# Performance work log

Measured on AMD Instinct MI355X. Metric: run time of the kernel, lower is better.

The kernel has to match this reference:

```python
import jax, jax.numpy as jnp
import numpy as np

N, F_NODE, F_FLOW, H, E, B, L = 131072, 64, 16, 128, 2097152, 256, 32


def setup_inputs() -> dict:
    key = jax.random.key(0)
    ks = jax.random.split(key, 24)
    gn = lambda k, s, sc: jax.random.normal(k, s, jnp.float32) * sc
    s_in = 1.0 / np.sqrt(F_NODE)
    s_h = 1.0 / np.sqrt(H)
    s_f = 1.0 / np.sqrt(F_FLOW)
    s_c = 1.0 / np.sqrt(2 * H + H // 2)
    inp = {
        "x": gn(ks[0], (N, F_NODE), 1.0),
        "edge_index": jax.random.randint(ks[1], (2, E), 0, N),
        "batch": jnp.sort(jax.random.randint(ks[2], (N,), 0, B)),
        "path_idx": jax.random.randint(ks[3], (B, L), 0, N),
        "path_len": jax.random.randint(ks[4], (B,), 1, L + 1),
        "flow": gn(ks[5], (B, F_FLOW), 1.0),
        # SAGEConv1: out = mean_agg(x_j) @ Wl.T + b + x_i @ Wr.T
        "Wl1": gn(ks[6], (H, F_NODE), s_in), "Wr1": gn(ks[7], (H, F_NODE), s_in), "b1": gn(ks[8], (H,), s_in),
        "Wl2": gn(ks[9], (H, H), s_h), "Wr2": gn(ks[10], (H, H), s_h), "b2": gn(ks[11], (H,), s_h),
        # LSTM (torch gate order i,f,g,o)
        "Wih": gn(ks[12], (4 * H, H), s_h), "Whh": gn(ks[13], (4 * H, H), s_h),
        "bih": gn(ks[14], (4 * H,), s_h), "bhh": gn(ks[15], (4 * H,), s_h),
        # flow encoder Linear(F_FLOW, H//2)
        "Wf": gn(ks[16], (H // 2, F_FLOW), s_f), "bf": gn(ks[17], (H // 2,), s_f),
        # scorer MLP: Linear(2H+H//2, H) -> ReLU -> Linear(H, 1)
        "Ws1": gn(ks[18], (H, 2 * H + H // 2), s_c), "bs1": gn(ks[19], (H,), s_c),
        "Ws2": gn(ks[20], (1, H), s_h), "bs2": gn(ks[21], (1,), s_h),
    }
    return inp


def _sage(x, src, dst, Wl, Wr, b, n):
    agg = jax.ops.segment_sum(x[src], dst, num_segments=n)  # [n, d]
    cnt = jax.ops.segment_sum(jnp.ones((src.shape[0],), x.dtype), dst, num_segments=n)
    mean = agg / jnp.maximum(cnt, 1.0)[:, None]
    return mean @ Wl.T + b + x @ Wr.T


def _lstm_final_h(seq, valid, Wih, Whh, bih, bhh):
    # seq: [B, L, H], valid: [B, L] bool; returns h at each path's last valid step
    b, l, h = seq.shape
    h0 = jnp.zeros((b, h), seq.dtype)

    def step(carry, inp):
        hp, cp = carry
        x_t, v = inp  # [B,H], [B]
        gates = x_t @ Wih.T + hp @ Whh.T + bih + bhh
        i, f, g, o = jnp.split(gates, 4, axis=-1)
        c_new = jax.nn.sigmoid(f) * cp + jax.nn.sigmoid(i) * jnp.tanh(g)
        h_new = jax.nn.sigmoid(o) * jnp.tanh(c_new)
        m = v[:, None]
        return (jnp.where(m, h_new, hp), jnp.where(m, c_new, cp)), None

    (hf, _), _ = jax.lax.scan(step, (h0, h0),
                              (jnp.swapaxes(seq, 0, 1), jnp.swapaxes(valid, 0, 1)))
    return hf


def reference(x, edge_index, batch, path_idx, path_len, flow,
              Wl1, Wr1, b1, Wl2, Wr2, b2,
              Wih, Whh, bih, bhh, Wf, bf, Ws1, bs1, Ws2, bs2):
    n = x.shape[0]
    src, dst = edge_index[0], edge_index[1]
    h1 = jax.nn.relu(_sage(x, src, dst, Wl1, Wr1, b1, n))
    node_emb = jax.nn.relu(_sage(h1, src, dst, Wl2, Wr2, b2, n))

    # global mean pool per graph
    gsum = jax.ops.segment_sum(node_emb, batch, num_segments=B)
    gcnt = jax.ops.segment_sum(jnp.ones((n,), node_emb.dtype), batch, num_segments=B)
    graph_emb = gsum / jnp.maximum(gcnt, 1.0)[:, None]  # [B, H]

    flow_emb = jax.nn.relu(flow @ Wf.T + bf)  # [B, H//2]

    path_seq = node_emb[path_idx]  # [B, L, H]
    valid = jnp.arange(L)[None, :] < path_len[:, None]  # [B, L]
    path_emb = _lstm_final_h(path_seq, valid, Wih, Whh, bih, bhh)  # [B, H]

    combined = jnp.concatenate([graph_emb, path_emb, flow_emb], axis=-1)
    hidden = jax.nn.relu(combined @ Ws1.T + bs1)
    scores = hidden @ Ws2.T + bs2  # [B, 1]
    return scores[:, 0]  # matches torch.cat of per-path [1] outputs -> [B]
```

## Files before the change

### kernel.cpp

```cpp
#include <hip/hip_runtime.h>
#include <hip/hip_bf16.h>

#define N_NODES 131072
#define N_EDGES 2097152
#define BATCHES 256
#define LPATH   32
#define NB   256
#define NPB  512
#define GB   256
#define EPB  8192

typedef __hip_bfloat16 bf16;
using short8  = __attribute__((ext_vector_type(8))) short;
using floatx4 = __attribute__((ext_vector_type(4))) float;

__device__ __forceinline__ float bl(unsigned u){ union {unsigned x; float f;} c; c.x = u << 16; return c.f; }
__device__ __forceinline__ float bh(unsigned u){ union {unsigned x; float f;} c; c.x = u & 0xffff0000u; return c.f; }
__device__ __forceinline__ unsigned packbf(float lo, float hi){
  bf16 l = __float2bfloat16(lo), h = __float2bfloat16(hi);
  unsigned short lu, hu;
  __builtin_memcpy(&lu, &l, 2); __builtin_memcpy(&hu, &h, 2);
  return (unsigned)lu | ((unsigned)hu << 16);
}
__device__ __forceinline__ float frcp(float x){ return __builtin_amdgcn_rcpf(x); }
__device__ __forceinline__ float sigf(float x){ return frcp(1.f + __expf(-x)); }
__device__ __forceinline__ float tanh_fast(float x){ return fmaf(2.f, frcp(1.f + __expf(-2.f * x)), -1.f); }

__global__ void prep_k(const float* __restrict__ Wl1, const float* __restrict__ Wr1,
                       const float* __restrict__ Wl2, const float* __restrict__ Wr2,
                       const float* __restrict__ Wih, const float* __restrict__ Whh,
                       const float* __restrict__ bih, const float* __restrict__ bhh,
                       bf16* __restrict__ Wcat1, bf16* __restrict__ Wcat2,
                       bf16* __restrict__ WihB, bf16* __restrict__ WhhB, float* __restrict__ bsumF){
  int g = blockIdx.x * 256 + threadIdx.x;
  if (g < 16384) {
    int h = g >> 7, k = g & 127;
    float v = (k < 64) ? Wl1[h * 64 + k] : Wr1[h * 64 + (k - 64)];
    Wcat1[g] = __float2bfloat16(v);
  } else if (g < 49152) {
    int q = g - 16384;
    int h = q >> 8, k = q & 255;
    float v = (k < 128) ? Wl2[h * 128 + k] : Wr2[h * 128 + (k - 128)];
    Wcat2[q] = __float2bfloat16(v);
  } else if (g < 114688) {
    int q = g - 49152;
    WihB[q] = __float2bfloat16(Wih[q]);
  } else if (g < 180224) {
    int q = g - 114688;
    WhhB[q] = __float2bfloat16(Whh[q]);
  } else if (g < 180736) {
    int k = g - 180224;
    bsumF[k] = bih[k] + bhh[k];
  }
}

__global__ void xb16_k(const float* __restrict__ x, bf16* __restrict__ xb, bf16* __restrict__ Acat1){
  int g = blockIdx.x * 256 + threadIdx.x;
  int n = g >> 5, p = g & 31;
  float2 v = *(const float2*)(x + (size_t)n * 64 + p * 2);
  unsigned u = packbf(v.x, v.y);
  *(unsigned*)(xb + (size_t)n * 64 + p * 2) = u;
  *(unsigned*)(Acat1 + (size_t)n * 128 + 64 + p * 2) = u;
}

__global__ void bounds_k(const int* __restrict__ batch, int* __restrict__ starts){
  int b = threadIdx.x;
  int lo = 0, hi = N_NODES;
  while (lo < hi){ int mid = (lo + hi) >> 1; if (batch[mid] < b) lo = mid + 1; else hi = mid; }
  starts[b] = lo;
  if (b == 0) starts[BATCHES] = N_NODES;
}

__global__ void cntA_k(const int* __restrict__ dst, int* __restrict__ cntA){
  __shared__ int h[NB];
  int tid = threadIdx.x;
  h[tid] = 0;
  __syncthreads();
  int base = blockIdx.x * EPB;
  #pragma unroll
  for (int i = 0; i < EPB / 256; ++i){
    int d = dst[base + i * 256 + tid];
    atomicAdd(&h[d >> 9], 1);
  }
  __syncthreads();
  cntA[tid * GB + blockIdx.x] = h[tid];
}

__global__ void scan1_k(const int* __restrict__ cnt, int* __restrict__ ofsA, int* __restrict__ bsum){
  __shared__ int sh[256];
  int t = threadIdx.x, i = blockIdx.x * 256 + t;
  int v = cnt[i];
  sh[t] = v; __syncthreads();
  int inc = v;
  for (int d = 1; d < 256; d <<= 1){
    int add = (t >= d) ? sh[t - d] : 0;
    __syncthreads();
    inc += add; sh[t] = inc;
    __syncthreads();
  }
  ofsA[i] = inc - v;
  if (t == 255) bsum[blockIdx.x] = inc;
}

__global__ void scan2_k(const int* __restrict__ bsum, int* __restrict__ bsumEx){
  __shared__ int sh[NB];
  int t = threadIdx.x;
  int v = bsum[t];
  sh[t] = v; __syncthreads();
  int inc = v;
  for (int d = 1; d < NB; d <<= 1){
    int add = (t >= d) ? sh[t - d] : 0;
    __syncthreads();
    inc += add; sh[t] = inc;
    __syncthreads();
  }
  bsumEx[t] = inc - v;
}

__global__ void passA2_k(const int* __restrict__ src, const int* __restrict__ dst,
                         const int* __restrict__ ofsA, const int* __restrict__ bsumEx,
                         unsigned* __restrict__ ebuf){
  __shared__ int cur[NB];
  int tid = threadIdx.x;
  cur[tid] = ofsA[tid * GB + blockIdx.x] + bsumEx[tid];
  __syncthreads();
  int base = blockIdx.x * EPB;
  #pragma unroll
  for (int i = 0; i < EPB / 256; ++i){
    int e = base + i * 256 + tid;
    int s = src[e], d = dst[e];
    int p = atomicAdd(&cur[d >> 9], 1);
    ebuf[p] = (unsigned)s | ((unsigned)(d & (NPB - 1)) << 17);
  }
}

__global__ void passB_k(const unsigned* __restrict__ ebuf, const int* __restrict__ bsumEx,
                        int* __restrict__ offs, int* __restrict__ srcS){
  __shared__ int ncnt[NPB];
  __shared__ int pairs[256];
  __shared__ int nofs[NPB];
  int k = blockIdx.x, tid = threadIdx.x;
  int bs = bsumEx[k];
  int be = (k < NB - 1) ? bsumEx[k + 1] : N_EDGES;
  ncnt[tid] = 0; ncnt[tid + 256] = 0;
  __syncthreads();
  for (int i = bs + tid; i < be; i += 256)
    atomicAdd(&ncnt[ebuf[i] >> 17], 1);
  __syncthreads();
  int p = ncnt[2 * tid] + ncnt[2 * tid + 1];
  pairs[tid] = p;
  __syncthreads();
  int inc = p;
  for (int d = 1; d < 256; d <<= 1){
    int add = (tid >= d) ? pairs[tid - d] : 0;
    __syncthreads();
    inc += add; pairs[tid] = inc;
    __syncthreads();
  }
  int ex = inc - p;
  nofs[2 * tid]     = ex;
  nofs[2 * tid + 1] = ex + ncnt[2 * tid];
  __syncthreads();
  offs[k * NPB + tid]       = bs + nofs[tid];
  offs[k * NPB + tid + 256] = bs + nofs[tid + 256];
  if (k == NB - 1 && tid == 0) offs[N_NODES] = N_EDGES;
  ncnt[tid] = nofs[tid]; ncnt[tid + 256] = nofs[tid + 256];
  __syncthreads();
  for (int i = bs + tid; i < be; i += 256){
    unsigned w = ebuf[i];
    int loc = w >> 17, sv = w & 0x1FFFF;
    int pp = atomicAdd(&ncnt[loc], 1);
    srcS[bs + pp] = sv;
  }
}

__global__ void agg1_k(const bf16* __restrict__ xb, const int* __restrict__ offs,
                       const int* __restrict__ srcS, bf16* __restrict__ Acat1){
  int wid = threadIdx.x >> 6, lane = threadIdx.x & 63;
  int n = blockIdx.x * 4 + wid;
  int s = offs[n], e = offs[n + 1];
  int slot = lane >> 3, fl = lane & 7;
  float a0=0,a1=0,a2=0,a3=0,a4=0,a5=0,a6=0,a7=0;
  float c0=0,c1=0,c2=0,c3=0,c4=0,c5=0,c6=0,c7=0;
  int i = s + slot;
  for (; i + 8 < e; i += 16){
    int sv0 = srcS[i], sv1 = srcS[i + 8];
    uint4 u = *(const uint4*)(xb + (size_t)sv0 * 64 + fl * 8);
    uint4 v = *(const uint4*)(xb + (size_t)sv1 * 64 + fl * 8);
    a0 += bl(u.x); a1 += bh(u.x); a2 += bl(u.y); a3 += bh(u.y);
    a4 += bl(u.z); a5 += bh(u.z); a6 += bl(u.w); a7 += bh(u.w);
    c0 += bl(v.x); c1 += bh(v.x); c2 += bl(v.y); c3 += bh(v.y);
    c4 += bl(v.z); c5 += bh(v.z); c6 += bl(v.w); c7 += bh(v.w);
  }
  if (i < e){
    int sv0 = srcS[i];
    uint4 u = *(const uint4*)(xb + (size_t)sv0 * 64 + fl * 8);
    a0 += bl(u.x); a1 += bh(u.x); a2 += bl(u.y); a3 += bh(u.y);
    a4 += bl(u.z); a5 += bh(u.z); a6 += bl(u.w); a7 += bh(u.w);
  }
  a0 += c0; a1 += c1; a2 += c2; a3 += c3;
  a4 += c4; a5 += c5; a6 += c6; a7 += c7;
  a0 += __shfl_xor(a0, 8); a0 += __shfl_xor(a0, 16); a0 += __shfl_xor(a0, 32);
  a1 += __shfl_xor(a1, 8); a1 += __shfl_xor(a1, 16); a1 += __shfl_xor(a1, 32);
  a2 += __shfl_xor(a2, 8); a2 += __shfl_xor(a2, 16); a2 += __shfl_xor(a2, 32);
  a3 += __shfl_xor(a3, 8); a3 += __shfl_xor(a3, 16); a3 += __shfl_xor(a3, 32);
  a4 += __shfl_xor(a4, 8); a4 += __shfl_xor(a4, 16); a4 += __shfl_xor(a4, 32);
  a5 += __shfl_xor(a5, 8); a5 += __shfl_xor(a5, 16); a5 += __shfl_xor(a5, 32);
  a6 += __shfl_xor(a6, 8); a6 += __shfl_xor(a6, 16); a6 += __shfl_xor(a6, 32);
  a7 += __shfl_xor(a7, 8); a7 += __shfl_xor(a7, 16); a7 += __shfl_xor(a7, 32);
  if (slot == 0){
    int d = e - s; if (d < 1) d = 1;
    float inv = 1.f / (float)d;
    uint4 w;
    w.x = packbf(a0 * inv, a1 * inv); w.y = packbf(a2 * inv, a3 * inv);
    w.z = packbf(a4 * inv, a5 * inv); w.w = packbf(a6 * inv, a7 * inv);
    *(uint4*)(Acat1 + (size_t)n * 128 + fl * 8) = w;
  }
}

__global__ void agg2_k(const int* __restrict__ offs, const int* __restrict__ srcS, bf16* __restrict__ Acat2){
  int wid = threadIdx.x >> 6, lane = threadIdx.x & 63;
  int n = blockIdx.x * 4 + wid;
  int s = offs[n], e = offs[n + 1];
  int slot = lane >> 4, fl = lane & 15;
  float a0=0,a1=0,a2=0,a3=0,a4=0,a5=0,a6=0,a7=0;
  float c0=0,c1=0,c2=0,c3=0,c4=0,c5=0,c6=0,c7=0;
  int i = s + slot;
  for (; i + 4 < e; i += 8){
    int sv0 = srcS[i], sv1 = srcS[i + 4];
    uint4 u = *(const uint4*)(Acat2 + (size_t)sv0 * 256 + 128 + fl * 8);
    uint4 v = *(const uint4*)(Acat2 + (size_t)sv1 * 256 + 128 + fl * 8);
    a0 += bl(u.x); a1 += bh(u.x); a2 += bl(u.y); a3 += bh(u.y);
    a4 += bl(u.z); a5 += bh(u.z); a6 += bl(u.w); a7 += bh(u.w);
    c0 += bl(v.x); c1 += bh(v.x); c2 += bl(v.y); c3 += bh(v.y);
    c4 += bl(v.z); c5 += bh(v.z); c6 += bl(v.w); c7 += bh(v.w);
  }
  if (i < e){
    int sv0 = srcS[i];
    uint4 u = *(const uint4*)(Acat2 + (size_t)sv0 * 256 + 128 + fl * 8);
    a0 += bl(u.x); a1 += bh(u.x); a2 += bl(u.y); a3 += bh(u.y);
    a4 += bl(u.z); a5 += bh(u.z); a6 += bl(u.w); a7 += bh(u.w);
  }
  a0 += c0; a1 += c1; a2 += c2; a3 += c3;
  a4 += c4; a5 += c5; a6 += c6; a7 += c7;
  a0 += __shfl_xor(a0, 16); a0 += __shfl_xor(a0, 32);
  a1 += __shfl_xor(a1, 16); a1 += __shfl_xor(a1, 32);
  a2 += __shfl_xor(a2, 16); a2 += __shfl_xor(a2, 32);
  a3 += __shfl_xor(a3, 16); a3 += __shfl_xor(a3, 32);
  a4 += __shfl_xor(a4, 16); a4 += __shfl_xor(a4, 32);
  a5 += __shfl_xor(a5, 16); a5 += __shfl_xor(a5, 32);
  a6 += __shfl_xor(a6, 16); a6 += __shfl_xor(a6, 32);
  a7 += __shfl_xor(a7, 16); a7 += __shfl_xor(a7, 32);
  if (slot == 0){
    int d = e - s; if (d < 1) d = 1;
    float inv = 1.f / (float)d;
    uint4 w;
    w.x = packbf(a0 * inv, a1 * inv); w.y = packbf(a2 * inv, a3 * inv);
    w.z = packbf(a4 * inv, a5 * inv); w.w = packbf(a6 * inv, a7 * inv);
    *(uint4*)(Acat2 + (size_t)n * 256 + fl * 8) = w;
  }
}

__global__ __launch_bounds__(256) void gemm_k(const bf16* __restrict__ A, int lda,
                                              const bf16* __restrict__ W, int K,
                                              const float* __restrict__ bias,
                                              void* __restrict__ out, int ldo, int outF32, int relu){
  __shared__ bf16 Wl[128][136];
  int tid = threadIdx.x;
  int wid = tid >> 6, lane = tid & 63;
  int l16 = lane & 15, quad = lane >> 4;
  int rowBase  = blockIdx.x * 64 + wid * 16;
  int colGroup = blockIdx.y * 128;
  floatx4 acc[8] = {};
  int nStage = K >> 7;
  for (int ks = 0; ks < nStage; ++ks){
    __syncthreads();
    for (int c = tid; c < 2048; c += 256){
      int r = c >> 4, kc = (c & 15) << 3;
      *(uint4*)(&Wl[r][kc]) = *(const uint4*)(W + (size_t)(colGroup + r) * K + ks * 128 + kc);
    }
    __syncthreads();
    for (int kk = 0; kk < 4; ++kk){
      short8 af = *(const short8*)(A + (size_t)(rowBase + l16) * lda + ks * 128 + kk * 32 + quad * 8);
      #pragma unroll
      for (int c = 0; c < 8; ++c){
        short8 bq = *(const short8*)(&Wl[c * 16 + l16][kk * 32 + quad * 8]);
        acc[c] = __builtin_amdgcn_mfma_f32_16x16x32_bf16(af, bq, acc[c], 0, 0, 0);
      }
    }
  }
  #pragma unroll
  for (int c = 0; c < 8; ++c){
    int col = colGroup + c * 16 + l16;
    float bv = bias ? bias[col] : 0.f;
    #pragma unroll
    for (int r = 0; r < 4; ++r){
      int row = rowBase + quad * 4 + r;
      float v = acc[c][r] + bv;
      if (relu) v = fmaxf(v, 0.f);
      if (outF32) ((float*)out)[(size_t)row * ldo + col] = v;
      else        ((bf16*)out)[(size_t)row * ldo + col]  = __float2bfloat16(v);
    }
  }
}

__global__ void pool_k(const bf16* __restrict__ ne, const int* __restrict__ starts, float* __restrict__ comb){
  __shared__ float sh[8][128];
  int b = blockIdx.x;
  int q = threadIdx.x >> 6, lane = threadIdx.x & 63;
  int s = starts[b], e = starts[b + 1];
  float a0 = 0.f, a1 = 0.f;
  for (int i = s + q; i < e; i += 8){
    unsigned u = *(const unsigned*)(ne + (size_t)i * 128 + lane * 2);
    a0 += bl(u); a1 += bh(u);
  }
  sh[q][lane * 2] = a0; sh[q][lane * 2 + 1] = a1;
  __syncthreads();
  if (threadIdx.x < 128){
    int f = threadIdx.x;
    float tot = 0.f;
    #pragma unroll
    for (int k = 0; k < 8; ++k) tot += sh[k][f];
    int d = e - s; if (d < 1) d = 1;
    comb[b * 320 + f] = tot / (float)d;
  }
}

__global__ void flow_k(const float* __restrict__ flow, const float* __restrict__ Wf,
                       const float* __restrict__ bfv, float* __restrict__ comb){
  int g = blockIdx.x * 256 + threadIdx.x;
  int b = g >> 6, j = g & 63;
  float acc = bfv[j];
  for (int k = 0; k < 16; ++k)
    acc += flow[b * 16 + k] * Wf[j * 16 + k];
  comb[b * 320 + 256 + j] = fmaxf(acc, 0.f);
}

__global__ void gather_k(const int* __restrict__ path_idx, const bf16* __restrict__ ne, bf16* __restrict__ ps){
  int wid = threadIdx.x >> 6, lane = threadIdx.x & 63;
  int r = blockIdx.x * 4 + wid;
  int idx = path_idx[r];
  ((unsigned*)ps)[(size_t)r * 64 + lane] = ((const unsigned*)ne)[(size_t)idx * 64 + lane];
}

__global__ __launch_bounds__(256, 1) void lstm_k(const bf16* __restrict__ Whh, const float* __restrict__ pre,
                                                 const int* __restrict__ path_len, float* __restrict__ comb){
  __shared__ bf16 hbuf[2][16][136];
  int tid = threadIdx.x;
  int w = tid >> 6, lane = tid & 63;
  int l16 = lane & 15, quad = lane >> 4;
  int b0 = blockIdx.x * 16;

  short8 wb[4][2][4];
  #pragma unroll
  for (int q = 0; q < 4; ++q)
    #pragma unroll
    for (int hf = 0; hf < 2; ++hf){
      const bf16* rp = Whh + (size_t)(q * 128 + w * 32 + hf * 16 + l16) * 128 + quad * 8;
      #pragma unroll
      for (int ks = 0; ks < 4; ++ks) wb[q][hf][ks] = *(const short8*)(rp + ks * 32);
    }

  int lenr[4];
  #pragma unroll
  for (int r = 0; r < 4; ++r){
    int L = path_len[b0 + quad * 4 + r];
    if (L < 1) L = 1; if (L > LPATH) L = LPATH;
    lenr[r] = L;
  }
  int maxlen = 1;
  for (int i = 0; i < 16; ++i){
    int L = path_len[b0 + i];
    if (L > LPATH) L = LPATH;
    if (L > maxlen) maxlen = L;
  }

  for (int i = tid; i < 1088; i += 256) ((unsigned*)&hbuf[0][0][0])[i] = 0;

  const float* pb[4];
  #pragma unroll
  for (int r = 0; r < 4; ++r)
    pb[r] = pre + (size_t)(b0 + quad * 4 + r) * LPATH * 512 + w * 32 + l16;

  float pv[4][2][4];
  #pragma unroll
  for (int q = 0; q < 4; ++q)
    #pragma unroll
    for (int hf = 0; hf < 2; ++hf)
      #pragma unroll
      for (int r = 0; r < 4; ++r)
        pv[q][hf][r] = pb[r][q * 128 + hf * 16];

  float cst[2][4] = {}, hst[2][4] = {};

  for (int t = 0; t < maxlen; ++t){
    int cur = t & 1, nxt = cur ^ 1;
    __syncthreads();
    short8 af[4];
    #pragma unroll
    for (int ks = 0; ks < 4; ++ks)
      af[ks] = *(const short8*)(&hbuf[cur][l16][ks * 32 + quad * 8]);
    int tn = (t + 1 < maxlen) ? t + 1 : t;
    float pnext[4][2][4];
    #pragma unroll
    for (int q = 0; q < 4; ++q)
      #pragma unroll
      for (int hf = 0; hf < 2; ++hf)
        #pragma unroll
        for (int r = 0; r < 4; ++r)
          pnext[q][hf][r] = pb[r][tn * 512 + q * 128 + hf * 16];
    floatx4 acc[4][2];
    #pragma unroll
    for (int q = 0; q < 4; ++q)
      #pragma unroll
      for (int hf = 0; hf < 2; ++hf){
        acc[q][hf][0] = pv[q][hf][0]; acc[q][hf][1] = pv[q][hf][1];
        acc[q][hf][2] = pv[q][hf][2]; acc[q][hf][3] = pv[q][hf][3];
      }
    #pragma unroll
    for (int ks = 0; ks < 4; ++ks)
      #pragma unroll
      for (int q = 0; q < 4; ++q)
        #pragma unroll
        for (int hf = 0; hf < 2; ++hf)
          acc[q][hf] = __builtin_amdgcn_mfma_f32_16x16x32_bf16(af[ks], wb[q][hf][ks], acc[q][hf], 0, 0, 0);
    #pragma unroll
    for (int hf = 0; hf < 2; ++hf)
      #pragma unroll
      for (int r = 0; r < 4; ++r){
        float ig = sigf(acc[0][hf][r]);
        float fg = sigf(acc[1][hf][r]);
        float gg = tanh_fast(acc[2][hf][r]);
        float og = sigf(acc[3][hf][r]);
        float cn = fmaf(fg, cst[hf][r], ig * gg);
        float hn = og * tanh_fast(cn);
        bool vld = t < lenr[r];
        cst[hf][r] = vld ? cn : cst[hf][r];
        hst[hf][r] = vld ? hn : hst[hf][r];
        hbuf[nxt][quad * 4 + r][w * 32 + hf * 16 + l16] = __float2bfloat16(hst[hf][r]);
      }
    #pragma unroll
    for (int q = 0; q < 4; ++q)
      #pragma unroll
      for (int hf = 0; hf < 2; ++hf)
        #pragma unroll
        for (int r = 0; r < 4; ++r)
          pv[q][hf][r] = pnext[q][hf][r];
  }

  #pragma unroll
  for (int hf = 0; hf < 2; ++hf)
    #pragma unroll
    for (int r = 0; r < 4; ++r)
      comb[(b0 + quad * 4 + r) * 320 + 128 + w * 32 + hf * 16 + l16] = hst[hf][r];
}

__global__ void head_k(const float* __restrict__ comb, const float* __restrict__ Ws1, const float* __restrict__ bs1,
                       const float* __restrict__ Ws2, const float* __restrict__ bs2, float* __restrict__ out){
  __shared__ float cl[320];
  __shared__ float red[128];
  int b = blockIdx.x, j = threadIdx.x;
  for (int k = j; k < 320; k += 128) cl[k] = comb[b * 320 + k];
  __syncthreads();
  float acc = bs1[j];
  const float4* wr = (const float4*)(Ws1 + (size_t)j * 320);
  #pragma unroll 4
  for (int kc = 0; kc < 80; ++kc){
    float4 u = wr[kc];
    int k = kc * 4;
    acc += u.x * cl[k] + u.y * cl[k + 1] + u.z * cl[k + 2] + u.w * cl[k + 3];
  }
  float hv = fmaxf(acc, 0.f);
  red[j] = hv * Ws2[j];
  __syncthreads();
  for (int s = 64; s > 0; s >>= 1){ if (j < s) red[j] += red[j + s]; __syncthreads(); }
  if (j == 0) out[b] = red[0] + bs2[0];
}

constexpr size_t OFF_OFFS   = 0;
constexpr size_t OFF_CNTA   = 524544;
constexpr size_t OFF_OFSA   = OFF_CNTA   + 262144;
constexpr size_t OFF_BSUM   = OFF_OFSA   + 262144;
constexpr size_t OFF_BSUMEX = OFF_BSUM   + 1024;
constexpr size_t OFF_STARTS = OFF_BSUMEX + 1024;
constexpr size_t OFF_SRCS   = OFF_STARTS + 2048;
constexpr size_t OFF_WCAT1  = OFF_SRCS   + 8388608;
constexpr size_t OFF_WCAT2  = OFF_WCAT1  + 32768;
constexpr size_t OFF_WIHB   = OFF_WCAT2  + 65536;
constexpr size_t OFF_WHHB   = OFF_WIHB   + 131072;
constexpr size_t OFF_BSUMF  = OFF_WHHB   + 131072;
constexpr size_t OFF_COMB   = OFF_BSUMF  + 2048;
constexpr size_t OFF_ACAT1  = OFF_COMB   + 327680;
constexpr size_t OFF_ACAT2  = OFF_ACAT1  + 33554432;
constexpr size_t OFF_EBUF   = OFF_ACAT2;
constexpr size_t OFF_PATHSEQ= OFF_ACAT2;
constexpr size_t OFF_PRE    = OFF_ACAT2  + 2097152;
constexpr size_t OFF_XB     = OFF_ACAT2  + 50331648;

extern "C" void kernel_launch(void* const* d_in, const int* in_sizes, int n_in,
                              void* d_out, int out_size, void* d_ws, size_t ws_size,
                              hipStream_t stream){
  const float* x      = (const float*)d_in[0];
  const int* edge     = (const int*)d_in[1];
  const int* batch    = (const int*)d_in[2];
  const int* path_idx = (const int*)d_in[3];
  const int* path_len = (const int*)d_in[4];
  const float* flow   = (const float*)d_in[5];
  const float* Wl1 = (const float*)d_in[6];
  const float* Wr1 = (const float*)d_in[7];
  const float* b1  = (const float*)d_in[8];
  const float* Wl2 = (const float*)d_in[9];
  const float* Wr2 = (const float*)d_in[10];
  const float* b2  = (const float*)d_in[11];
  const float* Wih = (const float*)d_in[12];
  const float* Whh = (const float*)d_in[13];
  const float* bih = (const float*)d_in[14];
  const float* bhh = (const float*)d_in[15];
  const float* Wf  = (const float*)d_in[16];
  const float* bfv = (const float*)d_in[17];
  const float* Ws1 = (const float*)d_in[18];
  const float* bs1 = (const float*)d_in[19];
  const float* Ws2 = (const float*)d_in[20];
  const float* bs2 = (const float*)d_in[21];

  char* ws = (char*)d_ws;
  int* offs    = (int*)(ws + OFF_OFFS);
  int* cntA    = (int*)(ws + OFF_CNTA);
  int* ofsA    = (int*)(ws + OFF_OFSA);
  int* bsum    = (int*)(ws + OFF_BSUM);
  int* bsumEx  = (int*)(ws + OFF_BSUMEX);
  int* starts  = (int*)(ws + OFF_STARTS);
  int* srcS    = (int*)(ws + OFF_SRCS);
  bf16* Wcat1  = (bf16*)(ws + OFF_WCAT1);
  bf16* Wcat2  = (bf16*)(ws + OFF_WCAT2);
  bf16* WihB   = (bf16*)(ws + OFF_WIHB);
  bf16* WhhB   = (bf16*)(ws + OFF_WHHB);
  float* bsumF = (float*)(ws + OFF_BSUMF);
  float* comb  = (float*)(ws + OFF_COMB);
  bf16* Acat1  = (bf16*)(ws + OFF_ACAT1);
  bf16* node_emb = Acat1;
  bf16* Acat2  = (bf16*)(ws + OFF_ACAT2);
  unsigned* ebuf = (unsigned*)(ws + OFF_EBUF);
  bf16* pathseq= (bf16*)(ws + OFF_PATHSEQ);
  float* pre   = (float*)(ws + OFF_PRE);
  bf16* xb     = (bf16*)(ws + OFF_XB);

  prep_k<<<707, 256, 0, stream>>>(Wl1, Wr1, Wl2, Wr2, Wih, Whh, bih, bhh, Wcat1, Wcat2, WihB, WhhB, bsumF);
  xb16_k<<<N_NODES / 8, 256, 0, stream>>>(x, xb, Acat1);
  bounds_k<<<1, 256, 0, stream>>>(batch, starts);
  cntA_k<<<GB, 256, 0, stream>>>(edge + N_EDGES, cntA);
  scan1_k<<<NB, 256, 0, stream>>>(cntA, ofsA, bsum);
  scan2_k<<<1, NB, 0, stream>>>(bsum, bsumEx);
  passA2_k<<<GB, 256, 0, stream>>>(edge, edge + N_EDGES, ofsA, bsumEx, ebuf);
  passB_k<<<NB, 256, 0, stream>>>(ebuf, bsumEx, offs, srcS);
  agg1_k<<<N_NODES / 4, 256, 0, stream>>>(xb, offs, srcS, Acat1);
  gemm_k<<<dim3(N_NODES / 64, 1), 256, 0, stream>>>(Acat1, 128, Wcat1, 128, b1, Acat2 + 128, 256, 0, 1);
  agg2_k<<<N_NODES / 4, 256, 0, stream>>>(offs, srcS, Acat2);
  gemm_k<<<dim3(N_NODES / 64, 1), 256, 0, stream>>>(Acat2, 256, Wcat2, 256, b2, node_emb, 128, 0, 1);
  pool_k<<<BATCHES, 512, 0, stream>>>(node_emb, starts, comb);
  flow_k<<<64, 256, 0, stream>>>(flow, Wf, bfv, comb);
  gather_k<<<BATCHES * LPATH / 4, 256, 0, stream>>>(path_idx, node_emb, pathseq);
  gemm_k<<<dim3(BATCHES * LPATH / 64, 4), 256, 0, stream>>>(pathseq, 128, WihB, 128, bsumF, pre, 512, 1, 0);
  lstm_k<<<BATCHES / 16, 256, 0, stream>>>(WhhB, pre, path_len, comb);
  head_k<<<BATCHES, 128, 0, stream>>>(comb, Ws1, bs1, Ws2, bs2, (float*)d_out);
}
```

Measured before the change: 458.4 us.

## Gather layer-2 neighbours from FP8 copy and fuse path gather into GEMM

A new kernel packs the layer-1 hidden features into an FP8 copy (128 bytes per node). The second aggregation then gathers neighbours from this copy instead of from bf16, which halves the bytes read in the random-access gather. Separately, the path gather kernel is removed and the LSTM input GEMM now indexes node_emb rows directly through path_idx. FP8 loses precision in the neighbour means and may push results past the tolerance, and the extra conversion pass adds a streaming read and write.

```diff
diff --git a/kernel.cpp b/kernel.cpp
--- a/kernel.cpp
+++ b/kernel.cpp
@@ -13,6 +13,7 @@
 typedef __hip_bfloat16 bf16;
 using short8  = __attribute__((ext_vector_type(8))) short;
 using floatx4 = __attribute__((ext_vector_type(4))) float;
+using floatx2 = __attribute__((ext_vector_type(2))) float;
 
 __device__ __forceinline__ float bl(unsigned u){ union {unsigned x; float f;} c; c.x = u << 16; return c.f; }
 __device__ __forceinline__ float bh(unsigned u){ union {unsigned x; float f;} c; c.x = u & 0xffff0000u; return c.f; }
@@ -218,59 +219,90 @@
   }
 }
 
-__global__ void agg2_k(const int* __restrict__ offs, const int* __restrict__ srcS, bf16* __restrict__ Acat2){
+__global__ void cvt8_k(const bf16* __restrict__ Acat2, unsigned* __restrict__ h1f8){
+  int g = blockIdx.x * 256 + threadIdx.x;
+  int n = g >> 5, p = g & 31;
+  uint2 u = *(const uint2*)(Acat2 + (size_t)n * 256 + 128 + p * 4);
+  int w = 0;
+  w = __builtin_amdgcn_cvt_pk_fp8_f32(bl(u.x), bh(u.x), w, false);
+  w = __builtin_amdgcn_cvt_pk_fp8_f32(bl(u.y), bh(u.y), w, true);
+  h1f8[(size_t)n * 32 + p] = (unsigned)w;
+}
+
+__global__ void agg2_k(const int* __restrict__ offs, const int* __restrict__ srcS,
+                       const unsigned* __restrict__ h1f8, bf16* __restrict__ Acat2){
   int wid = threadIdx.x >> 6, lane = threadIdx.x & 63;
   int n = blockIdx.x * 4 + wid;
   int s = offs[n], e = offs[n + 1];
-  int slot = lane >> 4, fl = lane & 15;
-  float a0=0,a1=0,a2=0,a3=0,a4=0,a5=0,a6=0,a7=0;
-  float c0=0,c1=0,c2=0,c3=0,c4=0,c5=0,c6=0,c7=0;
+  int slot = lane >> 3, fl = lane & 7;
+  float a[16] = {}, c[16] = {};
   int i = s + slot;
-  for (; i + 4 < e; i += 8){
-    int sv0 = srcS[i], sv1 = srcS[i + 4];
-    uint4 u = *(const uint4*)(Acat2 + (size_t)sv0 * 256 + 128 + fl * 8);
-    uint4 v = *(const uint4*)(Acat2 + (size_t)sv1 * 256 + 128 + fl * 8);
-    a0 += bl(u.x); a1 += bh(u.x); a2 += bl(u.y); a3 += bh(u.y);
-    a4 += bl(u.z); a5 += bh(u.z); a6 += bl(u.w); a7 += bh(u.w);
-    c0 += bl(v.x); c1 += bh(v.x); c2 += bl(v.y); c3 += bh(v.y);
-    c4 += bl(v.z); c5 += bh(v.z); c6 += bl(v.w); c7 += bh(v.w);
+  for (; i + 8 < e; i += 16){
+    int sv0 = srcS[i], sv1 = srcS[i + 8];
+    uint4 u = *(const uint4*)(h1f8 + (size_t)sv0 * 32 + fl * 4);
+    uint4 v = *(const uint4*)(h1f8 + (size_t)sv1 * 32 + fl * 4);
+    floatx2 p;
+    p = __builtin_amdgcn_cvt_pk_f32_fp8(u.x, false); a[0]+=p.x;  a[1]+=p.y;
+    p = __builtin_amdgcn_cvt_pk_f32_fp8(u.x, true);  a[2]+=p.x;  a[3]+=p.y;
+    p = __builtin_amdgcn_cvt_pk_f32_fp8(u.y, false); a[4]+=p.x;  a[5]+=p.y;
+    p = __builtin_amdgcn_cvt_pk_f32_fp8(u.y, true);  a[6]+=p.x;  a[7]+=p.y;
+    p = __builtin_amdgcn_cvt_pk_f32_fp8(u.z, false); a[8]+=p.x;  a[9]+=p.y;
+    p = __builtin_amdgcn_cvt_pk_f32_fp8(u.z, true);  a[10]+=p.x; a[11]+=p.y;
+    p = __builtin_amdgcn_cvt_pk_f32_fp8(u.w, false); a[12]+=p.x; a[13]+=p.y;
+    p = __builtin_amdgcn_cvt_pk_f32_fp8(u.w, true);  a[14]+=p.x; a[15]+=p.y;
+    p = __builtin_amdgcn_cvt_pk_f32_fp8(v.x, false); c[0]+=p.x;  c[1]+=p.y;
+    p = __builtin_amdgcn_cvt_pk_f32_fp8(v.x, true);  c[2]+=p.x;  c[3]+=p.y;
+    p = __builtin_amdgcn_cvt_pk_f32_fp8(v.y, false); c[4]+=p.x;  c[5]+=p.y;
+    p = __builtin_amdgcn_cvt_pk_f32_fp8(v.y, true);  c[6]+=p.x;  c[7]+=p.y;
+    p = __builtin_amdgcn_cvt_pk_f32_fp8(v.z, false); c[8]+=p.x;  c[9]+=p.y;
+    p = __builtin_amdgcn_cvt_pk_f32_fp8(v.z, true);  c[10]+=p.x; c[11]+=p.y;
+    p = __builtin_amdgcn_cvt_pk_f32_fp8(v.w, false); c[12]+=p.x; c[13]+=p.y;
+    p = __builtin_amdgcn_cvt_pk_f32_fp8(v.w, true);  c[14]+=p.x; c[15]+=p.y;
   }
   if (i < e){
     int sv0 = srcS[i];
-    uint4 u = *(const uint4*)(Acat2 + (size_t)sv0 * 256 + 128 + fl * 8);
-    a0 += bl(u.x); a1 += bh(u.x); a2 += bl(u.y); a3 += bh(u.y);
-    a4 += bl(u.z); a5 += bh(u.z); a6 += bl(u.w); a7 += bh(u.w);
-  }
-  a0 += c0; a1 += c1; a2 += c2; a3 += c3;
-  a4 += c4; a5 += c5; a6 += c6; a7 += c7;
-  a0 += __shfl_xor(a0, 16); a0 += __shfl_xor(a0, 32);
-  a1 += __shfl_xor(a1, 16); a1 += __shfl_xor(a1, 32);
-  a2 += __shfl_xor(a2, 16); a2 += __shfl_xor(a2, 32);
-  a3 += __shfl_xor(a3, 16); a3 += __shfl_xor(a3, 32);
-  a4 += __shfl_xor(a4, 16); a4 += __shfl_xor(a4, 32);
-  a5 += __shfl_xor(a5, 16); a5 += __shfl_xor(a5, 32);
-  a6 += __shfl_xor(a6, 16); a6 += __shfl_xor(a6, 32);
-  a7 += __shfl_xor(a7, 16); a7 += __shfl_xor(a7, 32);
+    uint4 u = *(const uint4*)(h1f8 + (size_t)sv0 * 32 + fl * 4);
+    floatx2 p;
+    p = __builtin_amdgcn_cvt_pk_f32_fp8(u.x, false); a[0]+=p.x;  a[1]+=p.y;
+    p = __builtin_amdgcn_cvt_pk_f32_fp8(u.x, true);  a[2]+=p.x;  a[3]+=p.y;
+    p = __builtin_amdgcn_cvt_pk_f32_fp8(u.y, false); a[4]+=p.x;  a[5]+=p.y;
+    p = __builtin_amdgcn_cvt_pk_f32_fp8(u.y, true);  a[6]+=p.x;  a[7]+=p.y;
+    p = __builtin_amdgcn_cvt_pk_f32_fp8(u.z, false); a[8]+=p.x;  a[9]+=p.y;
+    p = __builtin_amdgcn_cvt_pk_f32_fp8(u.z, true);  a[10]+=p.x; a[11]+=p.y;
+    p = __builtin_amdgcn_cvt_pk_f32_fp8(u.w, false); a[12]+=p.x; a[13]+=p.y;
+    p = __builtin_amdgcn_cvt_pk_f32_fp8(u.w, true);  a[14]+=p.x; a[15]+=p.y;
+  }
+  #pragma unroll
+  for (int j = 0; j < 16; ++j){
+    a[j] += c[j];
+    a[j] += __shfl_xor(a[j], 8); a[j] += __shfl_xor(a[j], 16); a[j] += __shfl_xor(a[j], 32);
+  }
   if (slot == 0){
     int d = e - s; if (d < 1) d = 1;
     float inv = 1.f / (float)d;
-    uint4 w;
-    w.x = packbf(a0 * inv, a1 * inv); w.y = packbf(a2 * inv, a3 * inv);
-    w.z = packbf(a4 * inv, a5 * inv); w.w = packbf(a6 * inv, a7 * inv);
-    *(uint4*)(Acat2 + (size_t)n * 256 + fl * 8) = w;
+    uint4 w0, w1;
+    w0.x = packbf(a[0] * inv,  a[1] * inv);  w0.y = packbf(a[2] * inv,  a[3] * inv);
+    w0.z = packbf(a[4] * inv,  a[5] * inv);  w0.w = packbf(a[6] * inv,  a[7] * inv);
+    w1.x = packbf(a[8] * inv,  a[9] * inv);  w1.y = packbf(a[10] * inv, a[11] * inv);
+    w1.z = packbf(a[12] * inv, a[13] * inv); w1.w = packbf(a[14] * inv, a[15] * inv);
+    *(uint4*)(Acat2 + (size_t)n * 256 + fl * 16)     = w0;
+    *(uint4*)(Acat2 + (size_t)n * 256 + fl * 16 + 8) = w1;
   }
 }
 
 __global__ __launch_bounds__(256) void gemm_k(const bf16* __restrict__ A, int lda,
                                               const bf16* __restrict__ W, int K,
                                               const float* __restrict__ bias,
-                                              void* __restrict__ out, int ldo, int outF32, int relu){
+                                              void* __restrict__ out, int ldo, int outF32, int relu,
+                                              const int* __restrict__ ridx){
   __shared__ bf16 Wl[128][136];
   int tid = threadIdx.x;
   int wid = tid >> 6, lane = tid & 63;
   int l16 = lane & 15, quad = lane >> 4;
   int rowBase  = blockIdx.x * 64 + wid * 16;
   int colGroup = blockIdx.y * 128;
+  int arow = rowBase + l16;
+  if (ridx) arow = ridx[arow];
   floatx4 acc[8] = {};
   int nStage = K >> 7;
   for (int ks = 0; ks < nStage; ++ks){
@@ -281,7 +313,7 @@
     }
     __syncthreads();
     for (int kk = 0; kk < 4; ++kk){
-      short8 af = *(const short8*)(A + (size_t)(rowBase + l16) * lda + ks * 128 + kk * 32 + quad * 8);
+      short8 af = *(const short8*)(A + (size_t)arow * lda + ks * 128 + kk * 32 + quad * 8);
       #pragma unroll
       for (int c = 0; c < 8; ++c){
         short8 bq = *(const short8*)(&Wl[c * 16 + l16][kk * 32 + quad * 8]);
@@ -334,13 +366,6 @@
   for (int k = 0; k < 16; ++k)
     acc += flow[b * 16 + k] * Wf[j * 16 + k];
   comb[b * 320 + 256 + j] = fmaxf(acc, 0.f);
-}
-
-__global__ void gather_k(const int* __restrict__ path_idx, const bf16* __restrict__ ne, bf16* __restrict__ ps){
-  int wid = threadIdx.x >> 6, lane = threadIdx.x & 63;
-  int r = blockIdx.x * 4 + wid;
-  int idx = path_idx[r];
-  ((unsigned*)ps)[(size_t)r * 64 + lane] = ((const unsigned*)ne)[(size_t)idx * 64 + lane];
 }
 
 __global__ __launch_bounds__(256, 1) void lstm_k(const bf16* __restrict__ Whh, const float* __restrict__ pre,
@@ -492,8 +517,8 @@
 constexpr size_t OFF_COMB   = OFF_BSUMF  + 2048;
 constexpr size_t OFF_ACAT1  = OFF_COMB   + 327680;
 constexpr size_t OFF_ACAT2  = OFF_ACAT1  + 33554432;
+constexpr size_t OFF_H1F8   = OFF_ACAT1;
 constexpr size_t OFF_EBUF   = OFF_ACAT2;
-constexpr size_t OFF_PATHSEQ= OFF_ACAT2;
 constexpr size_t OFF_PRE    = OFF_ACAT2  + 2097152;
 constexpr size_t OFF_XB     = OFF_ACAT2  + 50331648;
 
@@ -540,8 +565,8 @@
   bf16* Acat1  = (bf16*)(ws + OFF_ACAT1);
   bf16* node_emb = Acat1;
   bf16* Acat2  = (bf16*)(ws + OFF_ACAT2);
+  unsigned* h1f8 = (unsigned*)(ws + OFF_H1F8);
   unsigned* ebuf = (unsigned*)(ws + OFF_EBUF);
-  bf16* pathseq= (bf16*)(ws + OFF_PATHSEQ);
   float* pre   = (float*)(ws + OFF_PRE);
   bf16* xb     = (bf16*)(ws + OFF_XB);
 
@@ -554,13 +579,13 @@
   passA2_k<<<GB, 256, 0, stream>>>(edge, edge + N_EDGES, ofsA, bsumEx, ebuf);
   passB_k<<<NB, 256, 0, stream>>>(ebuf, bsumEx, offs, srcS);
   agg1_k<<<N_NODES / 4, 256, 0, stream>>>(xb, offs, srcS, Acat1);
-  gemm_k<<<dim3(N_NODES / 64, 1), 256, 0, stream>>>(Acat1, 128, Wcat1, 128, b1, Acat2 + 128, 256, 0, 1);
-  agg2_k<<<N_NODES / 4, 256, 0, stream>>>(offs, srcS, Acat2);
-  gemm_k<<<dim3(N_NODES / 64, 1), 256, 0, stream>>>(Acat2, 256, Wcat2, 256, b2, node_emb, 128, 0, 1);
+  gemm_k<<<dim3(N_NODES / 64, 1), 256, 0, stream>>>(Acat1, 128, Wcat1, 128, b1, Acat2 + 128, 256, 0, 1, nullptr);
+  cvt8_k<<<N_NODES / 8, 256, 0, stream>>>(Acat2, h1f8);
+  agg2_k<<<N_NODES / 4, 256, 0, stream>>>(offs, srcS, h1f8, Acat2);
+  gemm_k<<<dim3(N_NODES / 64, 1), 256, 0, stream>>>(Acat2, 256, Wcat2, 256, b2, node_emb, 128, 0, 1, nullptr);
   pool_k<<<BATCHES, 512, 0, stream>>>(node_emb, starts, comb);
   flow_k<<<64, 256, 0, stream>>>(flow, Wf, bfv, comb);
-  gather_k<<<BATCHES * LPATH / 4, 256, 0, stream>>>(path_idx, node_emb, pathseq);
-  gemm_k<<<dim3(BATCHES * LPATH / 64, 4), 256, 0, stream>>>(pathseq, 128, WihB, 128, bsumF, pre, 512, 1, 0);
+  gemm_k<<<dim3(BATCHES * LPATH / 64, 4), 256, 0, stream>>>(node_emb, 128, WihB, 128, bsumF, pre, 512, 1, 0, path_idx);
   lstm_k<<<BATCHES / 16, 256, 0, stream>>>(WhhB, pre, path_len, comb);
   head_k<<<BATCHES, 128, 0, stream>>>(comb, Ws1, bs1, Ws2, bs2, (float*)d_out);
 }
```

Result: no change. 463.4 us (+1.1%).
